# Kernel optimization log

Measured on AMD Instinct MI355X. Metric: run time of the kernel, lower is better.

Reference implementation:

```python
import jax, jax.numpy as jnp
import numpy as np


def _lstm(x, Wih, Whh, bih, bhh):
    # x: [B, T, D_in]; PyTorch gate order: i, f, g, o. Returns all hidden states [B, T, H].
    B = x.shape[0]
    H = Whh.shape[1]
    b = bih + bhh  # [4H]
    xs = jnp.transpose(x, (1, 0, 2))  # [T, B, D_in] for scan over time

    def step(carry, xt):
        h, c = carry
        gates = xt @ Wih.T + h @ Whh.T + b  # [B, 4H]
        i, f, g, o = jnp.split(gates, 4, axis=-1)
        i = jax.nn.sigmoid(i)
        f = jax.nn.sigmoid(f)
        g = jnp.tanh(g)
        o = jax.nn.sigmoid(o)
        c = f * c + i * g
        h = o * jnp.tanh(c)
        return (h, c), h

    h0 = jnp.zeros((B, H), dtype=x.dtype)
    c0 = jnp.zeros((B, H), dtype=x.dtype)
    _, hs = jax.lax.scan(step, (h0, c0), xs)  # hs: [T, B, H]
    return jnp.transpose(hs, (1, 0, 2))  # [B, T, H]


def setup_inputs() -> dict:
    key = jax.random.key(0)
    ks = jax.random.split(key, 11)
    B, T, D_IN, H1, H2, NC = 256, 2048, 16, 5, 50, 20

    def u(k, shape, fan):
        bound = 1.0 / np.sqrt(fan)
        return jax.random.uniform(k, shape, jnp.float32, -bound, bound)

    x = jax.random.normal(ks[0], (B, T, D_IN), dtype=jnp.float32)
    return {
        "x": x,
        "W1ih": u(ks[1], (4 * H1, D_IN), H1),
        "W1hh": u(ks[2], (4 * H1, H1), H1),
        "b1ih": u(ks[3], (4 * H1,), H1),
        "b1hh": u(ks[4], (4 * H1,), H1),
        "W2ih": u(ks[5], (4 * H2, H1), H2),
        "W2hh": u(ks[6], (4 * H2, H2), H2),
        "b2ih": u(ks[7], (4 * H2,), H2),
        "b2hh": u(ks[8], (4 * H2,), H2),
        "Wfc": u(ks[9], (NC, H2), H2),
        "bfc": u(ks[10], (NC,), H2),
    }


def reference(x, W1ih, W1hh, b1ih, b1hh, W2ih, W2hh, b2ih, b2hh, Wfc, bfc):
    h1 = _lstm(x, W1ih, W1hh, b1ih, b1hh)      # [B, T, 5]
    h2 = _lstm(h1, W2ih, W2hh, b2ih, b2hh)     # [B, T, 50]
    # Dropout(p=0.2) in eval mode == identity (deterministic reference)
    last = h2[:, -1, :]                        # [B, 50]
    result = last @ Wfc.T + bfc                # [B, num_classes]
    return (result, last)
```

## Files before the change

### kernel.cpp

```cpp
#include <hip/hip_runtime.h>
#include <math.h>

namespace {

constexpr int TSEQ   = 2048;
constexpr int DIN    = 16;
constexpr int NH1    = 5;
constexpr int NH2    = 50;
constexpr int NCLS   = 20;
constexpr int CHUNK  = 64;
constexpr int NCHUNK = TSEQ / CHUNK;
constexpr int BATCH  = 256;
constexpr int GSTR   = 80;
constexpr int PROW   = 4 * GSTR;

__device__ __forceinline__ float fast_sigm(float x) {
    return __fdividef(1.f, 1.f + __expf(-x));
}
__device__ __forceinline__ float fast_tanh(float x) {
    return fmaf(2.f, fast_sigm(2.f * x), -1.f);
}

template <int CTRL>
__device__ __forceinline__ float qperm(float v) {
    int i = __builtin_bit_cast(int, v);
    int r = __builtin_amdgcn_update_dpp(i, i, CTRL, 0xf, 0xf, false);
    return __builtin_bit_cast(float, r);
}
__device__ __forceinline__ float rdlane(float v, int lane) {
    return __builtin_bit_cast(float,
        __builtin_amdgcn_readlane(__builtin_bit_cast(int, v), lane));
}

__global__ __launch_bounds__(320, 1) void lstm_fused_kernel(
    const float* __restrict__ x,
    const float* __restrict__ W1ih,
    const float* __restrict__ W1hh,
    const float* __restrict__ b1ih,
    const float* __restrict__ b1hh,
    const float* __restrict__ W2ih,
    const float* __restrict__ W2hh,
    const float* __restrict__ b2ih,
    const float* __restrict__ b2hh,
    const float* __restrict__ Wfc,
    const float* __restrict__ bfc,
    float* __restrict__ out)
{
    const int b    = blockIdx.x;
    const int tid  = threadIdx.x;
    const int lane = tid & 63;
    const int wv   = tid >> 6;

    __shared__ __align__(16) float s_x[2][CHUNK * DIN];
    __shared__ __align__(16) float s_part[2][4][PROW];
    __shared__ __align__(16) float s_h1[2][CHUNK][8];
    __shared__ float s_h2[NH2];

    const float* xb = x + (size_t)b * TSEQ * DIN;

    const int r1 = (lane < NCLS) ? ((lane & 3) * NH1 + (lane >> 2)) : 0;
    float w1h[NH1], w1x[DIN];
    #pragma unroll
    for (int j = 0; j < NH1; ++j) w1h[j] = W1hh[r1 * NH1 + j];
    #pragma unroll
    for (int d = 0; d < DIN; ++d) w1x[d] = W1ih[r1 * DIN + d];
    const float bias1 = b1ih[r1] + b1hh[r1];
    const bool  isg1  = ((lane & 3) == 2) && (lane < NCLS);
    const float isc1  = isg1 ? 2.f : 1.f;
    const float osc1  = isg1 ? 2.f : 1.f;
    const float off1  = isg1 ? -1.f : 0.f;
    float c1 = 0.f;
    float sh0v = 0.f, sh1v = 0.f, sh2v = 0.f, sh3v = 0.f, sh4v = 0.f;
    float4 xr0, xr1, xr2, xr3;

    float wpw[4][13];
    #pragma unroll
    for (int i = 0; i < 4; ++i) {
        const int pr = 4 * lane + i;
        const int pg = pr >> 6;
        const int pu = pr & 63;
        #pragma unroll
        for (int kk = 0; kk < 13; ++kk) {
            const int k = wv * 13 + kk;
            wpw[i][kk] = (wv < 4 && pu < NH2 && k < NH2)
                       ? W2hh[(pg * NH2 + pu) * NH2 + k] : 0.f;
        }
    }

    const int  ul    = lane >> 2;
    const int  g     = lane & 3;
    const bool onc   = (ul < 13);
    const int  u     = (wv < 4 ? wv : 0) * 13 + (onc ? ul : 0);
    const bool ureal = (wv < 4) && onc && (u < NH2);
    float w2i[NH1];
    float bias2 = 0.f;
    if (ureal) {
        const int rr = g * NH2 + u;
        #pragma unroll
        for (int d = 0; d < NH1; ++d) w2i[d] = W2ih[rr * NH1 + d];
        bias2 = b2ih[rr] + b2hh[rr];
    } else {
        #pragma unroll
        for (int d = 0; d < NH1; ++d) w2i[d] = 0.f;
    }
    const bool  isg2 = (g == 2);
    const float isc2 = isg2 ? 2.f : 1.f;
    const float osc2 = isg2 ? 2.f : 1.f;
    const float off2 = isg2 ? -1.f : 0.f;

    const int wvc = (wv < 4) ? wv : 0;
    float4* wpart = (float4*)(&s_part[0][wvc][GSTR * (lane >> 4)]) + (lane & 15);
    const int crow = g * GSTR + u;
    const float* rpart = &s_part[0][0][crow];

    float hsl[13];
    #pragma unroll
    for (int k = 0; k < 13; ++k) hsl[k] = 0.f;
    float c2 = 0.f;

    auto l1_prod = [&](const float* xs, float* h1out) {
        float4 xv0 = *(const float4*)(xs + 0);
        float4 xv1 = *(const float4*)(xs + 4);
        float4 xv2 = *(const float4*)(xs + 8);
        float4 xv3 = *(const float4*)(xs + 12);
        float s = xv0.x * w1x[0];
        s = fmaf(xv0.y, w1x[1], s);  s = fmaf(xv0.z, w1x[2], s);
        s = fmaf(xv0.w, w1x[3], s);  s = fmaf(xv1.x, w1x[4], s);
        s = fmaf(xv1.y, w1x[5], s);  s = fmaf(xv1.z, w1x[6], s);
        s = fmaf(xv1.w, w1x[7], s);  s = fmaf(xv2.x, w1x[8], s);
        s = fmaf(xv2.y, w1x[9], s);  s = fmaf(xv2.z, w1x[10], s);
        s = fmaf(xv2.w, w1x[11], s); s = fmaf(xv3.x, w1x[12], s);
        s = fmaf(xv3.y, w1x[13], s); s = fmaf(xv3.z, w1x[14], s);
        s = fmaf(xv3.w, w1x[15], s);
        float g1 = s + bias1;
        g1 = fmaf(sh0v, w1h[0], g1); g1 = fmaf(sh1v, w1h[1], g1);
        g1 = fmaf(sh2v, w1h[2], g1); g1 = fmaf(sh3v, w1h[3], g1);
        g1 = fmaf(sh4v, w1h[4], g1);
        float act = fmaf(osc1, fast_sigm(isc1 * g1), off1);
        float f_ = qperm<0xB1>(act);
        float gg = qperm<0x4E>(act);
        float o_ = qperm<0x1B>(act);
        c1 = fmaf(f_, c1, act * gg);
        float h1me = o_ * fast_tanh(c1);
        sh0v = rdlane(h1me, 0);  sh1v = rdlane(h1me, 4);
        sh2v = rdlane(h1me, 8);  sh3v = rdlane(h1me, 12);
        sh4v = rdlane(h1me, 16);
        if (g == 0 && lane < NCLS) h1out[lane >> 2] = h1me;
    };

    if (wv == 4) {
        xr0 = ((const float4*)(xb))[lane];
        xr1 = ((const float4*)(xb + 256))[lane];
        xr2 = ((const float4*)(xb + 512))[lane];
        xr3 = ((const float4*)(xb + 768))[lane];
        ((float4*)s_x[0])[lane]       = xr0;
        ((float4*)s_x[0])[64 + lane]  = xr1;
        ((float4*)s_x[0])[128 + lane] = xr2;
        ((float4*)s_x[0])[192 + lane] = xr3;
        for (int t = 0; t < CHUNK; ++t)
            l1_prod(&s_x[0][t * DIN], &s_h1[0][t][0]);
        xr0 = ((const float4*)(xb + 1024))[lane];
        xr1 = ((const float4*)(xb + 1280))[lane];
        xr2 = ((const float4*)(xb + 1536))[lane];
        xr3 = ((const float4*)(xb + 1792))[lane];
        ((float4*)s_x[1])[lane]       = xr0;
        ((float4*)s_x[1])[64 + lane]  = xr1;
        ((float4*)s_x[1])[128 + lane] = xr2;
        ((float4*)s_x[1])[192 + lane] = xr3;
        xr0 = ((const float4*)(xb + 2048))[lane];
        xr1 = ((const float4*)(xb + 2304))[lane];
        xr2 = ((const float4*)(xb + 2560))[lane];
        xr3 = ((const float4*)(xb + 2816))[lane];
    }
    __syncthreads();

    float4 h1a = make_float4(0.f, 0.f, 0.f, 0.f);
    float  h1e = 0.f;

    #pragma unroll 1
    for (int c = 0; c < NCHUNK; ++c) {
        const int  cur   = c & 1, nxt = cur ^ 1;
        const bool w4run = (wv == 4) && (c + 1 < NCHUNK);

        if (wv == 4 && c + 2 < NCHUNK) {
            ((float4*)s_x[cur])[lane]       = xr0;
            ((float4*)s_x[cur])[64 + lane]  = xr1;
            ((float4*)s_x[cur])[128 + lane] = xr2;
            ((float4*)s_x[cur])[192 + lane] = xr3;
            if (c + 3 < NCHUNK) {
                const float* xc = xb + (size_t)(c + 3) * (CHUNK * DIN);
                xr0 = ((const float4*)(xc))[lane];
                xr1 = ((const float4*)(xc + 256))[lane];
                xr2 = ((const float4*)(xc + 512))[lane];
                xr3 = ((const float4*)(xc + 768))[lane];
            }
        }

        #define L2_PART(BUF, TT)                                               \
            if (wv < 4) {                                                      \
                h1a = *(const float4*)(&s_h1[cur][TT][0]);   \
                h1e = s_h1[cur][TT][4];                      \
                float a0 = 0.f, a1 = 0.f, a2 = 0.f, a3 = 0.f;                  \
                _Pragma("unroll")                                              \
                for (int kk = 0; kk < 13; ++kk) {                              \
                    a0 = fmaf(hsl[kk], wpw[0][kk], a0);                        \
                    a1 = fmaf(hsl[kk], wpw[1][kk], a1);                        \
                    a2 = fmaf(hsl[kk], wpw[2][kk], a2);                        \
                    a3 = fmaf(hsl[kk], wpw[3][kk], a3);                        \
                }                                                              \
                wpart[(BUF) * PROW] = make_float4(a0, a1, a2, a3);             \
            } else if (w4run) {                                                \
                l1_prod(&s_x[nxt][(TT) * DIN], &s_h1[nxt][TT][0]);             \
            }

        #define L2_COMB(BUF)                                                   \
            if (wv < 4) {                                                      \
                const float p0 = rpart[(BUF) * (4 * PROW) + 0 * PROW];         \
                const float p1 = rpart[(BUF) * (4 * PROW) + 1 * PROW];         \
                const float p2 = rpart[(BUF) * (4 * PROW) + 2 * PROW];         \
                const float p3 = rpart[(BUF) * (4 * PROW) + 3 * PROW];         \
                float pre = ((p0 + p1) + (p2 + p3)) + bias2;                   \
                pre = fmaf(h1a.x, w2i[0], pre);                                \
                pre = fmaf(h1a.y, w2i[1], pre);                                \
                pre = fmaf(h1a.z, w2i[2], pre);                                \
                pre = fmaf(h1a.w, w2i[3], pre);                                \
                pre = fmaf(h1e,  w2i[4], pre);                                 \
                float act2 = fmaf(osc2, fast_sigm(isc2 * pre), off2);          \
                float v1 = qperm<0xB1>(act2);                                  \
                float v2 = qperm<0x4E>(act2);                                  \
                float v3 = qperm<0x1B>(act2);                                  \
                c2 = fmaf(v1, c2, act2 * v2);                                  \
                float hn = v3 * fast_tanh(c2);                                 \
                _Pragma("unroll")                                              \
                for (int k = 0; k < 13; ++k) hsl[k] = rdlane(hn, 4 * k);       \
            }

        #pragma unroll 1
        for (int tt = 0; tt < CHUNK; tt += 2) {
            L2_PART(0, tt)
            __syncthreads();
            L2_COMB(0)
            L2_PART(1, tt + 1)
            __syncthreads();
            L2_COMB(1)
        }
        #undef L2_PART
        #undef L2_COMB
    }

    if (wv < 4) {
        float hv = 0.f;
        #pragma unroll
        for (int j = 0; j < 13; ++j)
            if (ul == j) hv = hsl[j];
        if (g == 0 && ureal) s_h2[u] = hv;
    }
    __syncthreads();

    if (tid < NH2) out[BATCH * NCLS + b * NH2 + tid] = s_h2[tid];
    if (tid < NCLS) {
        float acc = bfc[tid];
        const float* wr = Wfc + tid * NH2;
        #pragma unroll
        for (int j = 0; j < NH2; ++j) acc = fmaf(s_h2[j], wr[j], acc);
        out[b * NCLS + tid] = acc;
    }
}

}

extern "C" void kernel_launch(void* const* d_in, const int* in_sizes, int n_in,
                              void* d_out, int out_size, void* d_ws, size_t ws_size,
                              hipStream_t stream) {
    (void)in_sizes; (void)n_in; (void)d_ws; (void)ws_size; (void)out_size;
    const float* x    = (const float*)d_in[0];
    const float* W1ih = (const float*)d_in[1];
    const float* W1hh = (const float*)d_in[2];
    const float* b1ih = (const float*)d_in[3];
    const float* b1hh = (const float*)d_in[4];
    const float* W2ih = (const float*)d_in[5];
    const float* W2hh = (const float*)d_in[6];
    const float* b2ih = (const float*)d_in[7];
    const float* b2hh = (const float*)d_in[8];
    const float* Wfc  = (const float*)d_in[9];
    const float* bfc  = (const float*)d_in[10];

    lstm_fused_kernel<<<dim3(BATCH), dim3(320), 0, stream>>>(
        x, W1ih, W1hh, b1ih, b1hh, W2ih, W2hh, b2ih, b2hh, Wfc, bfc,
        (float*)d_out);
}
```

Measured before the change: 944.2 us.

## Shorten LSTM recurrence critical path with lighter barriers, hoisted input term, wave priority

After: 1.032 ms. +9.3%, slower.

```diff
diff --git a/kernel.cpp b/kernel.cpp
--- a/kernel.cpp
+++ b/kernel.cpp
@@ -31,6 +31,8 @@
     return __builtin_bit_cast(float,
         __builtin_amdgcn_readlane(__builtin_bit_cast(int, v), lane));
 }
+
+#define STEP_BARRIER() asm volatile("s_waitcnt lgkmcnt(0)\n\ts_barrier" ::: "memory")
 
 __global__ __launch_bounds__(320, 1) void lstm_fused_kernel(
     const float* __restrict__ x,
@@ -123,19 +125,18 @@
         float4 xv1 = *(const float4*)(xs + 4);
         float4 xv2 = *(const float4*)(xs + 8);
         float4 xv3 = *(const float4*)(xs + 12);
-        float s = xv0.x * w1x[0];
-        s = fmaf(xv0.y, w1x[1], s);  s = fmaf(xv0.z, w1x[2], s);
-        s = fmaf(xv0.w, w1x[3], s);  s = fmaf(xv1.x, w1x[4], s);
-        s = fmaf(xv1.y, w1x[5], s);  s = fmaf(xv1.z, w1x[6], s);
-        s = fmaf(xv1.w, w1x[7], s);  s = fmaf(xv2.x, w1x[8], s);
-        s = fmaf(xv2.y, w1x[9], s);  s = fmaf(xv2.z, w1x[10], s);
-        s = fmaf(xv2.w, w1x[11], s); s = fmaf(xv3.x, w1x[12], s);
-        s = fmaf(xv3.y, w1x[13], s); s = fmaf(xv3.z, w1x[14], s);
-        s = fmaf(xv3.w, w1x[15], s);
-        float g1 = s + bias1;
-        g1 = fmaf(sh0v, w1h[0], g1); g1 = fmaf(sh1v, w1h[1], g1);
-        g1 = fmaf(sh2v, w1h[2], g1); g1 = fmaf(sh3v, w1h[3], g1);
-        g1 = fmaf(sh4v, w1h[4], g1);
+        float sa = fmaf(xv0.y, w1x[1],  xv0.x * w1x[0]);
+        sa = fmaf(xv0.z, w1x[2], sa);  sa = fmaf(xv0.w, w1x[3], sa);
+        float sb = fmaf(xv1.y, w1x[5],  xv1.x * w1x[4]);
+        sb = fmaf(xv1.z, w1x[6], sb);  sb = fmaf(xv1.w, w1x[7], sb);
+        float sc = fmaf(xv2.y, w1x[9],  xv2.x * w1x[8]);
+        sc = fmaf(xv2.z, w1x[10], sc); sc = fmaf(xv2.w, w1x[11], sc);
+        float sd = fmaf(xv3.y, w1x[13], xv3.x * w1x[12]);
+        sd = fmaf(xv3.z, w1x[14], sd); sd = fmaf(xv3.w, w1x[15], sd);
+        float ha = fmaf(sh1v, w1h[1], sh0v * w1h[0]);
+        ha = fmaf(sh2v, w1h[2], ha);
+        float hb = fmaf(sh4v, w1h[4], sh3v * w1h[3]);
+        float g1 = ((sa + sb) + (sc + sd)) + ((ha + hb) + bias1);
         float act = fmaf(osc1, fast_sigm(isc1 * g1), off1);
         float f_ = qperm<0xB1>(act);
         float gg = qperm<0x4E>(act);
@@ -147,6 +148,8 @@
         sh4v = rdlane(h1me, 16);
         if (g == 0 && lane < NCLS) h1out[lane >> 2] = h1me;
     };
+
+    if (wv < 4) __builtin_amdgcn_s_setprio(1);
 
     if (wv == 4) {
         xr0 = ((const float4*)(xb))[lane];
@@ -172,10 +175,11 @@
         xr2 = ((const float4*)(xb + 2560))[lane];
         xr3 = ((const float4*)(xb + 2816))[lane];
     }
-    __syncthreads();
+    STEP_BARRIER();
 
     float4 h1a = make_float4(0.f, 0.f, 0.f, 0.f);
     float  h1e = 0.f;
+    float  xp  = 0.f;
 
     #pragma unroll 1
     for (int c = 0; c < NCHUNK; ++c) {
@@ -200,6 +204,11 @@
             if (wv < 4) {                                                      \
                 h1a = *(const float4*)(&s_h1[cur][TT][0]);   \
                 h1e = s_h1[cur][TT][4];                      \
+                xp = fmaf(h1a.x, w2i[0], bias2);                               \
+                xp = fmaf(h1a.y, w2i[1], xp);                                  \
+                xp = fmaf(h1a.z, w2i[2], xp);                                  \
+                xp = fmaf(h1a.w, w2i[3], xp);                                  \
+                xp = fmaf(h1e,  w2i[4], xp);                                   \
                 float a0 = 0.f, a1 = 0.f, a2 = 0.f, a3 = 0.f;                  \
                 _Pragma("unroll")                                              \
                 for (int kk = 0; kk < 13; ++kk) {                              \
@@ -219,12 +228,7 @@
                 const float p1 = rpart[(BUF) * (4 * PROW) + 1 * PROW];         \
                 const float p2 = rpart[(BUF) * (4 * PROW) + 2 * PROW];         \
                 const float p3 = rpart[(BUF) * (4 * PROW) + 3 * PROW];         \
-                float pre = ((p0 + p1) + (p2 + p3)) + bias2;                   \
-                pre = fmaf(h1a.x, w2i[0], pre);                                \
-                pre = fmaf(h1a.y, w2i[1], pre);                                \
-                pre = fmaf(h1a.z, w2i[2], pre);                                \
-                pre = fmaf(h1a.w, w2i[3], pre);                                \
-                pre = fmaf(h1e,  w2i[4], pre);                                 \
+                float pre = ((p0 + p1) + (p2 + p3)) + xp;                      \
                 float act2 = fmaf(osc2, fast_sigm(isc2 * pre), off2);          \
                 float v1 = qperm<0xB1>(act2);                                  \
                 float v2 = qperm<0x4E>(act2);                                  \
@@ -238,10 +242,10 @@
         #pragma unroll 1
         for (int tt = 0; tt < CHUNK; tt += 2) {
             L2_PART(0, tt)
-            __syncthreads();
+            STEP_BARRIER();
             L2_COMB(0)
             L2_PART(1, tt + 1)
-            __syncthreads();
+            STEP_BARRIER();
             L2_COMB(1)
         }
         #undef L2_PART
```
